# Optimization experiments

Hardware: AMD Instinct MI355X
Metric: run time of the kernel (lower is better)

## Reference

```python
import jax, jax.numpy as jnp
import numpy as np

N_NODES = 50000
N_EDGES = 800000
D_IN = 512
D_OUT = 512


def setup_inputs() -> dict:
    key = jax.random.key(0)
    k1, k2, k3, k4, k5 = jax.random.split(key, 5)
    x = jax.random.normal(k1, (N_NODES, D_IN), dtype=jnp.float32)
    weight = jax.random.normal(k2, (D_IN, D_OUT), dtype=jnp.float32) * (1.0 / np.sqrt(D_IN))
    edge_weight = jax.random.uniform(k3, (N_EDGES,), dtype=jnp.float32)
    edge_src = jax.random.randint(k4, (N_EDGES,), 0, N_NODES, dtype=jnp.int32)
    edge_dst = jax.random.randint(k5, (N_EDGES,), 0, N_NODES, dtype=jnp.int32)
    return {"x": x, "weight": weight, "edge_weight": edge_weight,
            "edge_src": edge_src, "edge_dst": edge_dst}


def reference(x, weight, edge_weight, edge_src, edge_dst):
    # support = x @ W  (dense GEMM, [N, D_out])
    support = jnp.matmul(x, weight)
    # output = adj @ support  (SpMM in COO form):
    # gather source rows, scale by edge weight, scatter-add into destinations
    msgs = support[edge_src] * edge_weight[:, None]          # [E, D_out]
    output = jax.ops.segment_sum(msgs, edge_dst, num_segments=N_NODES)
    return output
```

## Files before the change

### kernel.cpp

```cpp
#include <hip/hip_runtime.h>
#include <stdint.h>

#define N_NODES 50000
#define N_EDGES 800000
#define D 512
#define M_PAD 50048
#define CAP 64
#define CAPSH 6

#define WT_NB   1024
#define GEMM_NB 1564
#define FILL_NB 3125

typedef __attribute__((ext_vector_type(8))) __bf16 bf16x8;
typedef __attribute__((ext_vector_type(4))) float f32x4;

static __device__ __forceinline__ unsigned short f2bf(float f) {
  unsigned u = __float_as_uint(f);
  u += 0x7fff + ((u >> 16) & 1);
  return (unsigned short)(u >> 16);
}
static __device__ __forceinline__ float bf2f(unsigned short h) {
  return __uint_as_float(((unsigned)h) << 16);
}

static __device__ __forceinline__ void gload_lds16(const void* g, void* l) {
  __builtin_amdgcn_global_load_lds((const __attribute__((address_space(1))) unsigned*)g,
                                   (__attribute__((address_space(3))) unsigned*)l, 16, 0, 0);
}

__global__ __launch_bounds__(256) void k_pre(const float* __restrict__ w,
                                             unsigned short* __restrict__ wt,
                                             int* __restrict__ cur) {
  int t = blockIdx.x * 256 + threadIdx.x;
  if (t < N_NODES) cur[t] = 0;
  int n = blockIdx.x >> 1;
  int k = ((blockIdx.x & 1) << 8) + threadIdx.x;
  wt[n * D + k] = f2bf(w[k * D + n]);
}

__global__ __launch_bounds__(256) void k_gf(const float* __restrict__ X,
                                            const unsigned short* __restrict__ Bt,
                                            unsigned short* __restrict__ C,
                                            const float* __restrict__ ew,
                                            const int* __restrict__ esrc,
                                            const int* __restrict__ edst,
                                            int* __restrict__ cur,
                                            int2* __restrict__ cew) {
  __shared__ float          lds_af[128 * 32];
  __shared__ unsigned short lds_b [128 * 32];

  if (blockIdx.x >= GEMM_NB) {
    int e = (blockIdx.x - GEMM_NB) * 256 + threadIdx.x;
    int d = edst[e];
    int r = atomicAdd(&cur[d], 1);
    if (r < CAP) cew[(d << CAPSH) + r] = make_int2(esrc[e], __float_as_int(ew[e]));
    return;
  }

  const int orig = blockIdx.x;
  const int q = GEMM_NB / 8, rq = GEMM_NB % 8;
  const int xcd = orig & 7, jj0 = orig >> 3;
  const int wgid = (xcd < rq ? xcd * (q + 1) : rq * (q + 1) + (xcd - rq) * q) + jj0;
  const int bm = wgid >> 2, bn = wgid & 3;

  const int tid  = threadIdx.x;
  const int m0   = bm * 128, n0 = bn * 128;
  const int wave = tid >> 6, lane = tid & 63;
  const int wm   = wave & 1, wn = wave >> 1;
  const int l15  = lane & 15, quad = lane >> 4;

  f32x4 acc[4][4];
#pragma unroll
  for (int i = 0; i < 4; i++)
#pragma unroll
    for (int j = 0; j < 4; j++) acc[i][j] = f32x4{0.f, 0.f, 0.f, 0.f};

  for (int kt = 0; kt < D / 32; ++kt) {
    const int k0 = kt * 32;
    __syncthreads();
#pragma unroll
    for (int c = 0; c < 2; c++) {
      int i = c * 256 + wave * 64 + lane;
      int r = i >> 2, s = i & 3;
      int g = s ^ (r & 3);
      gload_lds16(&Bt[(long long)(n0 + r) * D + k0 + (g << 3)], &lds_b[(c * 256 + wave * 64) * 8]);
    }
#pragma unroll
    for (int c = 0; c < 4; c++) {
      int i = c * 256 + wave * 64 + lane;
      int r = i >> 3, s = i & 7;
      int g = s ^ (r & 7);
      int arow = m0 + r;
      arow = (arow < N_NODES) ? arow : (N_NODES - 1);
      gload_lds16(&X[(long long)arow * D + k0 + (g << 2)], &lds_af[(c * 256 + wave * 64) * 4]);
    }
    __syncthreads();
    bf16x8 af[4], bfr[4];
#pragma unroll
    for (int t = 0; t < 4; t++) {
      int ra = wm * 64 + t * 16 + l15;
      int ma = ra & 7;
      int c0 = quad * 2;
      f32x4 lo = *(const f32x4*)&lds_af[ra * 32 + ((c0 ^ ma) << 2)];
      f32x4 hi = *(const f32x4*)&lds_af[ra * 32 + (((c0 + 1) ^ ma) << 2)];
      bf16x8 a;
      a[0] = (__bf16)lo[0]; a[1] = (__bf16)lo[1]; a[2] = (__bf16)lo[2]; a[3] = (__bf16)lo[3];
      a[4] = (__bf16)hi[0]; a[5] = (__bf16)hi[1]; a[6] = (__bf16)hi[2]; a[7] = (__bf16)hi[3];
      af[t] = a;
      int rb = wn * 64 + t * 16 + l15;
      bfr[t] = *(const bf16x8*)&lds_b[rb * 32 + ((quad ^ (rb & 3)) << 3)];
    }
#pragma unroll
    for (int i = 0; i < 4; i++)
#pragma unroll
      for (int j = 0; j < 4; j++)
        acc[i][j] = __builtin_amdgcn_mfma_f32_16x16x32_bf16(af[i], bfr[j], acc[i][j], 0, 0, 0);
  }

#pragma unroll
  for (int i = 0; i < 4; i++)
#pragma unroll
    for (int j = 0; j < 4; j++)
#pragma unroll
      for (int r = 0; r < 4; r++) {
        int row = m0 + wm * 64 + i * 16 + quad * 4 + r;
        int col = n0 + wn * 64 + j * 16 + l15;
        C[(long long)row * D + col] = f2bf(acc[i][j][r]);
      }
}

__global__ __launch_bounds__(256) void k_agg(const int* __restrict__ cur,
                                             const int2* __restrict__ cew,
                                             const unsigned short* __restrict__ S,
                                             float* __restrict__ out) {
  __shared__ float s_part[4 * 512];
  const int node  = blockIdx.x;
  int cnt = cur[node];
  cnt = (cnt > CAP) ? CAP : cnt;
  const int start = node << CAPSH, end = start + cnt;
  const int wave  = threadIdx.x >> 6, lane = threadIdx.x & 63;
  float a[8];
#pragma unroll
  for (int k = 0; k < 8; k++) a[k] = 0.f;

#define EDGE_FMA(V, W)                                             \
  do {                                                             \
    a[0] = fmaf(W, bf2f((unsigned short)(V.x & 0xffffu)), a[0]);   \
    a[1] = fmaf(W, bf2f((unsigned short)(V.x >> 16)),     a[1]);   \
    a[2] = fmaf(W, bf2f((unsigned short)(V.y & 0xffffu)), a[2]);   \
    a[3] = fmaf(W, bf2f((unsigned short)(V.y >> 16)),     a[3]);   \
    a[4] = fmaf(W, bf2f((unsigned short)(V.z & 0xffffu)), a[4]);   \
    a[5] = fmaf(W, bf2f((unsigned short)(V.z >> 16)),     a[5]);   \
    a[6] = fmaf(W, bf2f((unsigned short)(V.w & 0xffffu)), a[6]);   \
    a[7] = fmaf(W, bf2f((unsigned short)(V.w >> 16)),     a[7]);   \
  } while (0)

#define GATHER(P) (*(const uint4*)(S + (size_t)(P).x * D + lane * 8))

  int e = start + wave;
  for (; e + 4 < end; e += 8) {
    int2 p0 = cew[e], p1 = cew[e + 4];
    uint4 v0 = GATHER(p0);
    uint4 v1 = GATHER(p1);
    EDGE_FMA(v0, __int_as_float(p0.y));
    EDGE_FMA(v1, __int_as_float(p1.y));
  }
  if (e < end) {
    int2 p0 = cew[e];
    uint4 v0 = GATHER(p0);
    EDGE_FMA(v0, __int_as_float(p0.y));
  }
#undef GATHER
#undef EDGE_FMA

  float4* sp = (float4*)&s_part[wave * 512 + lane * 8];
  sp[0] = make_float4(a[0], a[1], a[2], a[3]);
  sp[1] = make_float4(a[4], a[5], a[6], a[7]);
  __syncthreads();
  int col = threadIdx.x * 2;
  float2 r0 = *(const float2*)&s_part[0 * 512 + col];
  float2 r1 = *(const float2*)&s_part[1 * 512 + col];
  float2 r2 = *(const float2*)&s_part[2 * 512 + col];
  float2 r3 = *(const float2*)&s_part[3 * 512 + col];
  float2 res = make_float2(r0.x + r1.x + r2.x + r3.x, r0.y + r1.y + r2.y + r3.y);
  typedef __attribute__((ext_vector_type(2))) float f32x2;
  f32x2 rv = {res.x, res.y};
  __builtin_nontemporal_store(rv, (f32x2*)(out + (size_t)node * D + col));
}

extern "C" void kernel_launch(void* const* d_in, const int* in_sizes, int n_in,
                              void* d_out, int out_size, void* d_ws, size_t ws_size,
                              hipStream_t stream) {
  const float* x    = (const float*)d_in[0];
  const float* w    = (const float*)d_in[1];
  const float* ew   = (const float*)d_in[2];
  const int*   esrc = (const int*)d_in[3];
  const int*   edst = (const int*)d_in[4];
  float* out = (float*)d_out;

  char* p = (char*)d_ws;
  auto align256 = [](size_t v) { return (v + 255) & ~(size_t)255; };
  unsigned short* sb = (unsigned short*)p;  p += align256((size_t)M_PAD * D * 2);
  unsigned short* wt = (unsigned short*)p;  p += align256((size_t)D * D * 2);
  int*   cur  = (int*)p;   p += align256((size_t)N_NODES * 4);
  int2*  cew  = (int2*)p;  p += align256((size_t)N_NODES * CAP * 8);

  k_pre<<<WT_NB, 256, 0, stream>>>(w, wt, cur);
  k_gf<<<GEMM_NB + FILL_NB, 256, 0, stream>>>(x, wt, sb, ew, esrc, edst, cur, cew);
  k_agg<<<N_NODES, 256, 0, stream>>>(cur, cew, sb, out);
}
```

Measured before the change: 369.6 us.

## Double-buffer GEMM LDS tiles and change B-tile swizzle pattern

Splits the GEMM's LDS staging into two buffers. The next K-tile is loaded asynchronously with global_load_lds while MFMAs run on the current one, and one barrier per iteration is dropped. It also changes the XOR swizzle for the bf16 B tile to use (row>>1)&3, to cut LDS bank conflicts on 16-byte reads. LDS use doubles to about 48KB per block, which may lower occupancy. The single barrier placed after compute may not guarantee that the async loads have completed before they are read.

```diff
diff --git a/kernel.cpp b/kernel.cpp
--- a/kernel.cpp
+++ b/kernel.cpp
@@ -47,8 +47,8 @@
                                             const int* __restrict__ edst,
                                             int* __restrict__ cur,
                                             int2* __restrict__ cew) {
-  __shared__ float          lds_af[128 * 32];
-  __shared__ unsigned short lds_b [128 * 32];
+  __shared__ float          lds_af[2][128 * 32];
+  __shared__ unsigned short lds_b [2][128 * 32];
 
   if (blockIdx.x >= GEMM_NB) {
     int e = (blockIdx.x - GEMM_NB) * 256 + threadIdx.x;
@@ -76,47 +76,58 @@
 #pragma unroll
     for (int j = 0; j < 4; j++) acc[i][j] = f32x4{0.f, 0.f, 0.f, 0.f};
 
+#define STAGE(KT, B)                                                                          \
+  do {                                                                                        \
+    const int k0_ = (KT) * 32;                                                                \
+    _Pragma("unroll")                                                                         \
+    for (int c = 0; c < 2; c++) {                \
+      int i = c * 256 + wave * 64 + lane;                                                     \
+      int r = i >> 2, s = i & 3;                                                              \
+      int g = s ^ ((r >> 1) & 3);                                                             \
+      gload_lds16(&Bt[(long long)(n0 + r) * D + k0_ + (g << 3)],                              \
+                  &lds_b[B][(c * 256 + wave * 64) * 8]);                                      \
+    }                                                                                         \
+    _Pragma("unroll")                                                                         \
+    for (int c = 0; c < 4; c++) {               \
+      int i = c * 256 + wave * 64 + lane;                                                     \
+      int r = i >> 3, s = i & 7;                                                              \
+      int g = s ^ (r & 7);                                                                    \
+      int arow = m0 + r;                                                                      \
+      arow = (arow < N_NODES) ? arow : (N_NODES - 1);           \
+      gload_lds16(&X[(long long)arow * D + k0_ + (g << 2)],                                   \
+                  &lds_af[B][(c * 256 + wave * 64) * 4]);                                     \
+    }                                                                                         \
+  } while (0)
+
+  STAGE(0, 0);
+  __syncthreads();
+
   for (int kt = 0; kt < D / 32; ++kt) {
-    const int k0 = kt * 32;
-    __syncthreads();
-#pragma unroll
-    for (int c = 0; c < 2; c++) {
-      int i = c * 256 + wave * 64 + lane;
-      int r = i >> 2, s = i & 3;
-      int g = s ^ (r & 3);
-      gload_lds16(&Bt[(long long)(n0 + r) * D + k0 + (g << 3)], &lds_b[(c * 256 + wave * 64) * 8]);
-    }
-#pragma unroll
-    for (int c = 0; c < 4; c++) {
-      int i = c * 256 + wave * 64 + lane;
-      int r = i >> 3, s = i & 7;
-      int g = s ^ (r & 7);
-      int arow = m0 + r;
-      arow = (arow < N_NODES) ? arow : (N_NODES - 1);
-      gload_lds16(&X[(long long)arow * D + k0 + (g << 2)], &lds_af[(c * 256 + wave * 64) * 4]);
-    }
-    __syncthreads();
+    const int cur_ = kt & 1;
+    if (kt + 1 < D / 32) STAGE(kt + 1, cur_ ^ 1);
     bf16x8 af[4], bfr[4];
 #pragma unroll
     for (int t = 0; t < 4; t++) {
       int ra = wm * 64 + t * 16 + l15;
       int ma = ra & 7;
       int c0 = quad * 2;
-      f32x4 lo = *(const f32x4*)&lds_af[ra * 32 + ((c0 ^ ma) << 2)];
-      f32x4 hi = *(const f32x4*)&lds_af[ra * 32 + (((c0 + 1) ^ ma) << 2)];
+      f32x4 lo = *(const f32x4*)&lds_af[cur_][ra * 32 + ((c0 ^ ma) << 2)];
+      f32x4 hi = *(const f32x4*)&lds_af[cur_][ra * 32 + (((c0 + 1) ^ ma) << 2)];
       bf16x8 a;
       a[0] = (__bf16)lo[0]; a[1] = (__bf16)lo[1]; a[2] = (__bf16)lo[2]; a[3] = (__bf16)lo[3];
       a[4] = (__bf16)hi[0]; a[5] = (__bf16)hi[1]; a[6] = (__bf16)hi[2]; a[7] = (__bf16)hi[3];
       af[t] = a;
       int rb = wn * 64 + t * 16 + l15;
-      bfr[t] = *(const bf16x8*)&lds_b[rb * 32 + ((quad ^ (rb & 3)) << 3)];
+      bfr[t] = *(const bf16x8*)&lds_b[cur_][rb * 32 + ((quad ^ ((rb >> 1) & 3)) << 3)];
     }
 #pragma unroll
     for (int i = 0; i < 4; i++)
 #pragma unroll
       for (int j = 0; j < 4; j++)
         acc[i][j] = __builtin_amdgcn_mfma_f32_16x16x32_bf16(af[i], bfr[j], acc[i][j], 0, 0, 0);
-  }
+    __syncthreads();
+  }
+#undef STAGE
 
 #pragma unroll
   for (int i = 0; i < 4; i++)
```

Measured after the change: 390.9 us. +5.7%, slower.
